# Kernel optimization log

Measured on AMD Instinct MI355X. Metric: run time of the kernel, lower is better.

Reference implementation:

```python
import jax, jax.numpy as jnp
import numpy as np

LN_EPS = 1e-5
SUM_EPS = 1e-6
Q_EPS = 1e-8

def layernorm(x):
    # parameter-free LayerNorm over last axis (elementwise_affine=False)
    mu = jnp.mean(x, axis=-1, keepdims=True)
    var = jnp.mean(jnp.square(x - mu), axis=-1, keepdims=True)
    return (x - mu) * jax.lax.rsqrt(var + LN_EPS)

def ternary_quant(W):
    # BitNet-b1.58-style ternary quantization: scale = mean(|W|), Wq in {-1,0,1}*scale
    scale = jnp.mean(jnp.abs(W))
    Wq = jnp.clip(jnp.round(W / (scale + Q_EPS)), -1.0, 1.0) * scale
    return Wq

def setup_inputs() -> dict:
    key = jax.random.key(0)
    ks = jax.random.split(key, 8)
    B, S, F = 8, 2048, 2048
    x = jax.random.normal(ks[0], (B, S, F), dtype=jnp.float32)
    seq_pos_code = jnp.arange(S, dtype=jnp.int32)
    feature_pos_code = jnp.arange(F, dtype=jnp.int32)
    # TernaryMLP(F, F, residual=False): ternary-quantized linear F -> F
    W_v = jax.random.normal(ks[1], (F, F), dtype=jnp.float32) * (1.0 / np.sqrt(F))
    b_v = jnp.zeros((F,), dtype=jnp.float32)
    # left attn: Linear(F, 1)
    w_left = jax.random.normal(ks[2], (F, 1), dtype=jnp.float32) * (1.0 / np.sqrt(F))
    b_left = jnp.zeros((1,), dtype=jnp.float32)
    # right attn: Linear(S, 1)
    w_right = jax.random.normal(ks[3], (S, 1), dtype=jnp.float32) * (1.0 / np.sqrt(S))
    b_right = jnp.zeros((1,), dtype=jnp.float32)
    alpha = jax.random.uniform(ks[4], (1,), dtype=jnp.float32)
    return {"x": x, "seq_pos_code": seq_pos_code, "feature_pos_code": feature_pos_code,
            "W_v": W_v, "b_v": b_v, "w_left": w_left, "b_left": b_left,
            "w_right": w_right, "b_right": b_right, "alpha": alpha}

def reference(x, seq_pos_code, feature_pos_code, W_v, b_v, w_left, b_left, w_right, b_right, alpha):
    B, S, F = x.shape
    # value path: ternary-quantized linear (TernaryMLP, residual=False)
    Wq = ternary_quant(W_v)
    v = jnp.einsum('bsf,fg->bsg', x, Wq) + b_v  # [B,S,F]
    # left attention: Linear(F->1) -> [B,S,1]; transpose; LN over S; ReLU; transpose back
    la = (jnp.einsum('bsf,fo->bso', x, w_left) + b_left)[..., 0]  # [B,S]
    la = jax.nn.relu(layernorm(la))[..., None]                    # [B,S,1]
    la = la / (jnp.sum(la, axis=-1, keepdims=True) + SUM_EPS)     # normalize over last dim (size 1)
    # right attention: transpose -> [B,F,S]; Linear(S->1); transpose -> [B,1,F]; LN over F; ReLU
    ra = (jnp.einsum('bsf,so->bfo', x, w_right) + b_right)[..., 0]  # [B,F]
    ra = jax.nn.relu(layernorm(ra))[:, None, :]                     # [B,1,F]
    ra = ra / (jnp.sum(ra, axis=-1, keepdims=True) + SUM_EPS)       # normalize over F
    a = alpha[0]
    return (1.0 - a) * x + a * la * v * ra
```

## Files before the change

### kernel.cpp

```cpp
#include <hip/hip_runtime.h>
#include <hip/hip_bf16.h>
#include <stdint.h>

#define B_ 8
#define S_ 2048
#define F_ 2048
#define M_ (B_*S_)
#define K_ F_
#define N_ F_

typedef __attribute__((ext_vector_type(4))) float f32x4;
typedef __attribute__((ext_vector_type(8))) short short8;

__device__ __forceinline__ unsigned short f2bf(float f){
  unsigned u = __float_as_uint(f);
  u += 0x7FFFu + ((u >> 16) & 1u);
  return (unsigned short)(u >> 16);
}

__device__ __forceinline__ void gload16(const void* g, const void* l){
  __builtin_amdgcn_global_load_lds(
      (const __attribute__((address_space(1))) void*)g,
      (__attribute__((address_space(3))) void*)l,
      16, 0, 0);
}

__device__ __forceinline__ float waveReduce(float v){
  #pragma unroll
  for (int off = 32; off; off >>= 1) v += __shfl_down(v, off, 64);
  return v;
}

__device__ __forceinline__ float blockReduceAll(float v, float* sbuf){
  v = waveReduce(v);
  int lane = threadIdx.x & 63, w = threadIdx.x >> 6;
  __syncthreads();
  if (lane == 0) sbuf[w] = v;
  __syncthreads();
  return sbuf[0] + sbuf[1] + sbuf[2] + sbuf[3];
}

__global__ __launch_bounds__(256) void k_abs1(const float* __restrict__ W, float* __restrict__ part){
  __shared__ float sb[4];
  size_t idx = ((size_t)blockIdx.x * 256 + threadIdx.x) * 4;
  f32x4 v = *(const f32x4*)(W + idx);
  float s = fabsf(v[0]) + fabsf(v[1]) + fabsf(v[2]) + fabsf(v[3]);
  s = blockReduceAll(s, sb);
  if (threadIdx.x == 0) part[blockIdx.x] = s;
}

__global__ __launch_bounds__(256) void k_abs2(const float* __restrict__ part, float* __restrict__ scalep){
  __shared__ float sb[4];
  float s = 0.f;
  int t = threadIdx.x;
  #pragma unroll
  for (int i = 0; i < 16; i++) s += part[t + i*256];
  s = blockReduceAll(s, sb);
  if (t == 0) scalep[0] = s * (1.0f / ((float)F_ * (float)F_));
}

__global__ __launch_bounds__(256) void k_quantT(const float* __restrict__ W, unsigned short* __restrict__ BT,
                                                const float* __restrict__ scalep){
  __shared__ float tile[32][33];
  int gx = blockIdx.x * 32;
  int fy = blockIdx.y * 32;
  int tx = threadIdx.x & 31, ty = threadIdx.x >> 5;
  float inv = 1.0f / (scalep[0] + 1e-8f);
  #pragma unroll
  for (int i = 0; i < 4; i++){
    int f = fy + ty + i*8;
    tile[ty + i*8][tx] = W[(size_t)f * F_ + gx + tx];
  }
  __syncthreads();
  #pragma unroll
  for (int i = 0; i < 4; i++){
    int g = gx + ty + i*8;
    float w = tile[tx][ty + i*8];
    float t = rintf(w * inv);
    t = fminf(1.0f, fmaxf(-1.0f, t));
    BT[(size_t)g * K_ + fy + tx] = f2bf(t);
  }
}

__global__ __launch_bounds__(256) void k_conv_la(const float* __restrict__ X, const float* __restrict__ wl,
                                                 const float* __restrict__ bl, unsigned short* __restrict__ XH,
                                                 float* __restrict__ la_raw){
  __shared__ float sb[4];
  int row = blockIdx.x;
  const float* xr = X + (size_t)row * F_;
  unsigned short* xh = XH + (size_t)row * F_;
  int t = threadIdx.x;
  float s = 0.f;
  #pragma unroll
  for (int i = 0; i < 2; i++){
    int base = t*4 + i*1024;
    f32x4 v  = *(const f32x4*)(xr + base);
    f32x4 wv = *(const f32x4*)(wl + base);
    s += v[0]*wv[0] + v[1]*wv[1] + v[2]*wv[2] + v[3]*wv[3];
    ushort4 p;
    p.x = f2bf(v[0]); p.y = f2bf(v[1]); p.z = f2bf(v[2]); p.w = f2bf(v[3]);
    *(ushort4*)(xh + base) = p;
  }
  s = blockReduceAll(s, sb);
  if (t == 0) la_raw[row] = s + bl[0];
}

__global__ __launch_bounds__(256) void k_ra(const float* __restrict__ X, const float* __restrict__ wrt,
                                            float* __restrict__ ra_raw){
  int f  = blockIdx.x * 256 + threadIdx.x;
  int b  = blockIdx.y;
  int s0 = blockIdx.z * 256;
  const float* xb = X + (size_t)b * S_ * F_ + (size_t)s0 * F_ + f;
  float acc = 0.f;
  #pragma unroll 8
  for (int s = 0; s < 256; ++s)
    acc += xb[(size_t)s * F_] * wrt[s0 + s];
  atomicAdd(&ra_raw[b * F_ + f], acc);
}

__global__ __launch_bounds__(256) void k_ln_la(const float* __restrict__ la_raw, float* __restrict__ la){
  __shared__ float sb[4];
  int b = blockIdx.x;
  const float* p = la_raw + b * S_;
  int t = threadIdx.x;
  float v[8]; float s = 0.f, s2 = 0.f;
  #pragma unroll
  for (int i = 0; i < 8; i++){ v[i] = p[t + i*256]; s += v[i]; s2 += v[i]*v[i]; }
  s  = blockReduceAll(s,  sb);
  s2 = blockReduceAll(s2, sb);
  float mu  = s * (1.0f / S_);
  float var = s2 * (1.0f / S_) - mu*mu;
  float rstd = 1.0f / sqrtf(var + 1e-5f);
  #pragma unroll
  for (int i = 0; i < 8; i++){
    float x = (v[i] - mu) * rstd;
    x = fmaxf(x, 0.0f);
    la[b * S_ + t + i*256] = x / (x + 1e-6f);
  }
}

__global__ __launch_bounds__(256) void k_ln_ra(const float* __restrict__ ra_raw, const float* __restrict__ br,
                                               float* __restrict__ ra){
  __shared__ float sb[4];
  int b = blockIdx.x;
  const float* p = ra_raw + b * F_;
  int t = threadIdx.x;
  float bb = br[0];
  float v[8]; float s = 0.f, s2 = 0.f;
  #pragma unroll
  for (int i = 0; i < 8; i++){ v[i] = p[t + i*256] + bb; s += v[i]; s2 += v[i]*v[i]; }
  s  = blockReduceAll(s,  sb);
  s2 = blockReduceAll(s2, sb);
  float mu  = s * (1.0f / F_);
  float var = s2 * (1.0f / F_) - mu*mu;
  float rstd = 1.0f / sqrtf(var + 1e-5f);
  float r[8]; float sr = 0.f;
  #pragma unroll
  for (int i = 0; i < 8; i++){ r[i] = fmaxf((v[i] - mu) * rstd, 0.0f); sr += r[i]; }
  sr = blockReduceAll(sr, sb);
  float invs = 1.0f / (sr + 1e-6f);
  #pragma unroll
  for (int i = 0; i < 8; i++) ra[b * F_ + t + i*256] = r[i] * invs;
}

__global__ __launch_bounds__(256) void k_gemm(
    const unsigned short* __restrict__ A, const unsigned short* __restrict__ BT,
    const float* __restrict__ X, const float* __restrict__ la, const float* __restrict__ ra,
    const float* __restrict__ bv, const float* __restrict__ alphap, const float* __restrict__ scalep,
    float* __restrict__ Out)
{
  __shared__ __align__(128) char lds[16384];
  const int NBX = N_ / 128;
  int tid = threadIdx.x;
  int bid = blockIdx.x;
  const int nwg = (M_/128) * (N_/128);
  int cpx = nwg >> 3;
  int swz = (bid & 7) * cpx + (bid >> 3);
  int brow = swz / NBX, bcol = swz % NBX;
  int row0 = brow * 128, col0 = bcol * 128;

  int w = tid >> 6, lane = tid & 63;
  int wr = w >> 1, wc = w & 1;
  int lrow = lane & 15, kgrp = lane >> 4;

  f32x4 acc[4][4];
  #pragma unroll
  for (int m = 0; m < 4; m++)
    #pragma unroll
    for (int n = 0; n < 4; n++) acc[m][n] = (f32x4)(0.0f);

  int c0 = tid, c1 = tid + 256;
  int ar0 = c0 >> 2, ak0 = (((c0 & 3) ^ (ar0 & 3)) << 3);
  int ar1 = c1 >> 2, ak1 = (((c1 & 3) ^ (ar1 & 3)) << 3);
  const unsigned short* Ap0 = A  + (size_t)(row0 + ar0) * K_ + ak0;
  const unsigned short* Ap1 = A  + (size_t)(row0 + ar1) * K_ + ak1;
  const unsigned short* Bp0 = BT + (size_t)(col0 + ar0) * K_ + ak0;
  const unsigned short* Bp1 = BT + (size_t)(col0 + ar1) * K_ + ak1;
  char* ldsA = lds;
  char* ldsB = lds + 8192;
  const void* dA0 = ldsA + w*1024;
  const void* dA1 = ldsA + 4096 + w*1024;
  const void* dB0 = ldsB + w*1024;
  const void* dB1 = ldsB + 4096 + w*1024;

  int aoff[4], boff[4];
  #pragma unroll
  for (int m = 0; m < 4; m++){
    int r  = wr*64 + m*16 + lrow;
    aoff[m] = r*64 + ((kgrp ^ (r & 3)) << 4);
    int rc = wc*64 + m*16 + lrow;
    boff[m] = rc*64 + ((kgrp ^ (rc & 3)) << 4);
  }

  for (int kt = 0; kt < K_/32; ++kt){
    gload16(Ap0, dA0); gload16(Ap1, dA1);
    gload16(Bp0, dB0); gload16(Bp1, dB1);
    Ap0 += 32; Ap1 += 32; Bp0 += 32; Bp1 += 32;
    asm volatile("s_waitcnt vmcnt(0)" ::: "memory");
    __syncthreads();
    short8 af[4], bf[4];
    #pragma unroll
    for (int m = 0; m < 4; m++) af[m] = *(const short8*)(ldsA + aoff[m]);
    #pragma unroll
    for (int n = 0; n < 4; n++) bf[n] = *(const short8*)(ldsB + boff[n]);
    #pragma unroll
    for (int m = 0; m < 4; m++)
      #pragma unroll
      for (int n = 0; n < 4; n++)
        acc[m][n] = __builtin_amdgcn_mfma_f32_16x16x32_bf16(af[m], bf[n], acc[m][n], 0, 0, 0);
    __syncthreads();
  }

  float a = alphap[0];
  float scale = scalep[0];
  float oma = 1.0f - a;
  int bidx = row0 >> 11;
  const float* rab = ra + bidx * F_;
  #pragma unroll
  for (int m = 0; m < 4; m++){
    int rbase = row0 + wr*64 + m*16 + (lane >> 4) * 4;
    float lav[4];
    #pragma unroll
    for (int r = 0; r < 4; r++) lav[r] = la[rbase + r];
    #pragma unroll
    for (int n = 0; n < 4; n++){
      int col = col0 + wc*64 + n*16 + (lane & 15);
      float rav = rab[col];
      float bvv = bv[col];
      #pragma unroll
      for (int r = 0; r < 4; r++){
        int row = rbase + r;
        float v = acc[m][n][r] * scale + bvv;
        size_t idx = (size_t)row * N_ + col;
        Out[idx] = oma * X[idx] + a * lav[r] * v * rav;
      }
    }
  }
}

extern "C" void kernel_launch(void* const* d_in, const int* in_sizes, int n_in,
                              void* d_out, int out_size, void* d_ws, size_t ws_size,
                              hipStream_t stream){
  const float* x     = (const float*)d_in[0];
  const float* Wv    = (const float*)d_in[3];
  const float* bv    = (const float*)d_in[4];
  const float* wl    = (const float*)d_in[5];
  const float* bl    = (const float*)d_in[6];
  const float* wrt   = (const float*)d_in[7];
  const float* br    = (const float*)d_in[8];
  const float* alpha = (const float*)d_in[9];
  float* out = (float*)d_out;

  char* ws = (char*)d_ws;
  unsigned short* XH = (unsigned short*)(ws);
  unsigned short* BT = (unsigned short*)(ws + 67108864);
  float* la_raw = (float*)(ws + 75497472);
  float* la     = (float*)(ws + 75563008);
  float* ra_raw = (float*)(ws + 75628544);
  float* ra     = (float*)(ws + 75694080);
  float* part   = (float*)(ws + 75759616);
  float* scalep = (float*)(ws + 75776000);

  hipMemsetAsync(ra_raw, 0, B_ * F_ * sizeof(float), stream);
  k_abs1<<<4096, 256, 0, stream>>>(Wv, part);
  k_abs2<<<1, 256, 0, stream>>>(part, scalep);
  k_quantT<<<dim3(F_/32, F_/32), 256, 0, stream>>>(Wv, BT, scalep);
  k_conv_la<<<M_, 256, 0, stream>>>(x, wl, bl, XH, la_raw);
  k_ra<<<dim3(F_/256, B_, S_/256), 256, 0, stream>>>(x, wrt, ra_raw);
  k_ln_la<<<B_, 256, 0, stream>>>(la_raw, la);
  k_ln_ra<<<B_, 256, 0, stream>>>(ra_raw, br, ra);
  k_gemm<<<2048, 256, 0, stream>>>(XH, BT, x, la, ra, bv, alpha, scalep, out);
}
```

Before: 510.4 us.

## Double-buffer GEMM LDS tiles and fuse front-end reductions into one pass

The GEMM main loop now uses two LDS stages, issuing the next K-tile's global-to-LDS loads before computing on the current one. The LDS swizzle changes to XOR on (row>>1) and MFMA issue priority is raised around the inner product. Separately, the bf16 conversion, the left-attention dot product and the right-attention column reduction are fused into one kernel, so x is read once for all three instead of twice. The cost is doubled LDS use per block, which can lower occupancy, and atomics on ra_raw from many blocks.

```diff
diff --git a/kernel.cpp b/kernel.cpp
--- a/kernel.cpp
+++ b/kernel.cpp
@@ -82,40 +82,46 @@
   }
 }
 
-__global__ __launch_bounds__(256) void k_conv_la(const float* __restrict__ X, const float* __restrict__ wl,
-                                                 const float* __restrict__ bl, unsigned short* __restrict__ XH,
-                                                 float* __restrict__ la_raw){
-  __shared__ float sb[4];
-  int row = blockIdx.x;
-  const float* xr = X + (size_t)row * F_;
-  unsigned short* xh = XH + (size_t)row * F_;
-  int t = threadIdx.x;
-  float s = 0.f;
-  #pragma unroll
-  for (int i = 0; i < 2; i++){
-    int base = t*4 + i*1024;
-    f32x4 v  = *(const f32x4*)(xr + base);
-    f32x4 wv = *(const f32x4*)(wl + base);
-    s += v[0]*wv[0] + v[1]*wv[1] + v[2]*wv[2] + v[3]*wv[3];
-    ushort4 p;
-    p.x = f2bf(v[0]); p.y = f2bf(v[1]); p.z = f2bf(v[2]); p.w = f2bf(v[3]);
-    *(ushort4*)(xh + base) = p;
-  }
-  s = blockReduceAll(s, sb);
-  if (t == 0) la_raw[row] = s + bl[0];
-}
-
-__global__ __launch_bounds__(256) void k_ra(const float* __restrict__ X, const float* __restrict__ wrt,
-                                            float* __restrict__ ra_raw){
-  int f  = blockIdx.x * 256 + threadIdx.x;
-  int b  = blockIdx.y;
-  int s0 = blockIdx.z * 256;
-  const float* xb = X + (size_t)b * S_ * F_ + (size_t)s0 * F_ + f;
-  float acc = 0.f;
-  #pragma unroll 8
-  for (int s = 0; s < 256; ++s)
-    acc += xb[(size_t)s * F_] * wrt[s0 + s];
-  atomicAdd(&ra_raw[b * F_ + f], acc);
+__global__ __launch_bounds__(256) void k_front(const float* __restrict__ X, const float* __restrict__ wl,
+                                               const float* __restrict__ bl, const float* __restrict__ wrt,
+                                               unsigned short* __restrict__ XH, float* __restrict__ la_raw,
+                                               float* __restrict__ ra_raw){
+  __shared__ float lap[4][32];
+  int t = threadIdx.x, w = t >> 6, lane = t & 63;
+  int r0 = blockIdx.x * 32;
+  int b  = r0 >> 11;
+  int f0 = t * 8;
+  f32x4 wl0 = *(const f32x4*)(wl + f0);
+  f32x4 wl1 = *(const f32x4*)(wl + f0 + 4);
+  float racc[8];
+  #pragma unroll
+  for (int j = 0; j < 8; j++) racc[j] = 0.f;
+
+  for (int rr = 0; rr < 32; ++rr){
+    int row = r0 + rr;
+    const float* xr = X + (size_t)row * F_ + f0;
+    f32x4 v0 = *(const f32x4*)(xr);
+    f32x4 v1 = *(const f32x4*)(xr + 4);
+    ushort4 p0, p1;
+    p0.x = f2bf(v0[0]); p0.y = f2bf(v0[1]); p0.z = f2bf(v0[2]); p0.w = f2bf(v0[3]);
+    p1.x = f2bf(v1[0]); p1.y = f2bf(v1[1]); p1.z = f2bf(v1[2]); p1.w = f2bf(v1[3]);
+    unsigned short* xh = XH + (size_t)row * F_ + f0;
+    *(ushort4*)(xh)     = p0;
+    *(ushort4*)(xh + 4) = p1;
+    float dot = v0[0]*wl0[0] + v0[1]*wl0[1] + v0[2]*wl0[2] + v0[3]*wl0[3]
+              + v1[0]*wl1[0] + v1[1]*wl1[1] + v1[2]*wl1[2] + v1[3]*wl1[3];
+    dot = waveReduce(dot);
+    if (lane == 0) lap[w][rr] = dot;
+    float wsr = wrt[row & (S_-1)];
+    racc[0] += v0[0]*wsr; racc[1] += v0[1]*wsr; racc[2] += v0[2]*wsr; racc[3] += v0[3]*wsr;
+    racc[4] += v1[0]*wsr; racc[5] += v1[1]*wsr; racc[6] += v1[2]*wsr; racc[7] += v1[3]*wsr;
+  }
+  __syncthreads();
+  if (t < 32)
+    la_raw[r0 + t] = lap[0][t] + lap[1][t] + lap[2][t] + lap[3][t] + bl[0];
+  float* rb = ra_raw + b * F_ + f0;
+  #pragma unroll
+  for (int j = 0; j < 8; j++) atomicAdd(&rb[j], racc[j]);
 }
 
 __global__ __launch_bounds__(256) void k_ln_la(const float* __restrict__ la_raw, float* __restrict__ la){
@@ -169,7 +175,7 @@
     const float* __restrict__ bv, const float* __restrict__ alphap, const float* __restrict__ scalep,
     float* __restrict__ Out)
 {
-  __shared__ __align__(128) char lds[16384];
+  __shared__ __align__(128) char lds[32768];
   const int NBX = N_ / 128;
   int tid = threadIdx.x;
   int bid = blockIdx.x;
@@ -190,45 +196,62 @@
     for (int n = 0; n < 4; n++) acc[m][n] = (f32x4)(0.0f);
 
   int c0 = tid, c1 = tid + 256;
-  int ar0 = c0 >> 2, ak0 = (((c0 & 3) ^ (ar0 & 3)) << 3);
-  int ar1 = c1 >> 2, ak1 = (((c1 & 3) ^ (ar1 & 3)) << 3);
+  int ar0 = c0 >> 2, ak0 = (((c0 & 3) ^ ((ar0 >> 1) & 3)) << 3);
+  int ar1 = c1 >> 2, ak1 = (((c1 & 3) ^ ((ar1 >> 1) & 3)) << 3);
   const unsigned short* Ap0 = A  + (size_t)(row0 + ar0) * K_ + ak0;
   const unsigned short* Ap1 = A  + (size_t)(row0 + ar1) * K_ + ak1;
   const unsigned short* Bp0 = BT + (size_t)(col0 + ar0) * K_ + ak0;
   const unsigned short* Bp1 = BT + (size_t)(col0 + ar1) * K_ + ak1;
-  char* ldsA = lds;
-  char* ldsB = lds + 8192;
-  const void* dA0 = ldsA + w*1024;
-  const void* dA1 = ldsA + 4096 + w*1024;
-  const void* dB0 = ldsB + w*1024;
-  const void* dB1 = ldsB + 4096 + w*1024;
+  int stoff = w * 1024;
 
   int aoff[4], boff[4];
   #pragma unroll
   for (int m = 0; m < 4; m++){
     int r  = wr*64 + m*16 + lrow;
-    aoff[m] = r*64 + ((kgrp ^ (r & 3)) << 4);
+    aoff[m] = r*64 + ((kgrp ^ ((r >> 1) & 3)) << 4);
     int rc = wc*64 + m*16 + lrow;
-    boff[m] = rc*64 + ((kgrp ^ (rc & 3)) << 4);
-  }
-
+    boff[m] = 8192 + rc*64 + ((kgrp ^ ((rc >> 1) & 3)) << 4);
+  }
+
+  {
+    char* base = lds;
+    gload16(Ap0, base + stoff);
+    gload16(Ap1, base + 4096 + stoff);
+    gload16(Bp0, base + 8192 + stoff);
+    gload16(Bp1, base + 12288 + stoff);
+  }
+  asm volatile("s_waitcnt vmcnt(0)" ::: "memory");
+  __syncthreads();
+
+  int cur = 0;
   for (int kt = 0; kt < K_/32; ++kt){
-    gload16(Ap0, dA0); gload16(Ap1, dA1);
-    gload16(Bp0, dB0); gload16(Bp1, dB1);
-    Ap0 += 32; Ap1 += 32; Bp0 += 32; Bp1 += 32;
-    asm volatile("s_waitcnt vmcnt(0)" ::: "memory");
-    __syncthreads();
-    short8 af[4], bf[4];
-    #pragma unroll
-    for (int m = 0; m < 4; m++) af[m] = *(const short8*)(ldsA + aoff[m]);
-    #pragma unroll
-    for (int n = 0; n < 4; n++) bf[n] = *(const short8*)(ldsB + boff[n]);
+    if (kt < K_/32 - 1){
+      char* nb = lds + (cur ^ 1) * 16384;
+      const unsigned short* a0 = Ap0 + (kt+1)*32;
+      const unsigned short* a1 = Ap1 + (kt+1)*32;
+      const unsigned short* b0 = Bp0 + (kt+1)*32;
+      const unsigned short* b1 = Bp1 + (kt+1)*32;
+      gload16(a0, nb + stoff);
+      gload16(a1, nb + 4096 + stoff);
+      gload16(b0, nb + 8192 + stoff);
+      gload16(b1, nb + 12288 + stoff);
+    }
+    const char* bb = lds + cur * 16384;
+    short8 af[4], bfr[4];
+    #pragma unroll
+    for (int m = 0; m < 4; m++) af[m]  = *(const short8*)(bb + aoff[m]);
+    #pragma unroll
+    for (int n = 0; n < 4; n++) bfr[n] = *(const short8*)(bb + boff[n]);
+    __builtin_amdgcn_s_setprio(1);
     #pragma unroll
     for (int m = 0; m < 4; m++)
       #pragma unroll
       for (int n = 0; n < 4; n++)
-        acc[m][n] = __builtin_amdgcn_mfma_f32_16x16x32_bf16(af[m], bf[n], acc[m][n], 0, 0, 0);
+        acc[m][n] = __builtin_amdgcn_mfma_f32_16x16x32_bf16(af[m], bfr[n], acc[m][n], 0, 0, 0);
+    __builtin_amdgcn_s_setprio(0);
+    asm volatile("s_waitcnt vmcnt(0)" ::: "memory");
     __syncthreads();
+    cur ^= 1;
   }
 
   float a = alphap[0];
@@ -285,8 +308,7 @@
   k_abs1<<<4096, 256, 0, stream>>>(Wv, part);
   k_abs2<<<1, 256, 0, stream>>>(part, scalep);
   k_quantT<<<dim3(F_/32, F_/32), 256, 0, stream>>>(Wv, BT, scalep);
-  k_conv_la<<<M_, 256, 0, stream>>>(x, wl, bl, XH, la_raw);
-  k_ra<<<dim3(F_/256, B_, S_/256), 256, 0, stream>>>(x, wrt, ra_raw);
+  k_front<<<M_/32, 256, 0, stream>>>(x, wl, bl, wrt, XH, la_raw, ra_raw);
   k_ln_la<<<B_, 256, 0, stream>>>(la_raw, la);
   k_ln_ra<<<B_, 256, 0, stream>>>(ra_raw, br, ra);
   k_gemm<<<2048, 256, 0, stream>>>(XH, BT, x, la, ra, bv, alpha, scalep, out);
```

New measurement: 527.0 us. 3.2% more time.
